# Performance work log

Hardware: AMD Instinct MI355X
Metric: run time of the kernel (lower is better)

## Reference

```python
import math
import jax, jax.numpy as jnp
import numpy as np

SR = 22050
FRAME_SIZE = 1025
MAX_FILTER_SIZE = 20
B, T = 16, 2048


def _build_transform_matrix(frame_size=FRAME_SIZE, sr=SR, max_filter_size=MAX_FILTER_SIZE):
    max_freq = sr / 2
    freq = np.linspace(0, max_freq, num=frame_size, endpoint=True)
    mel = 2595 * np.log10(1 + freq / 700)
    min_mel, max_mel = mel[0], mel[-1]
    raw = (mel - min_mel) / (max_mel - min_mel) * (max_filter_size - 1) + 1
    mtx = np.zeros((frame_size, frame_size), dtype=np.float32)
    for i in range(frame_size):
        fs = math.floor(raw[i]) // 2 * 2 + 1
        start, end = i - fs // 2, i + fs // 2 + 1
        start, end = max(0, start), min(end, frame_size)
        mtx[i, start:end] = 1.0 / (end - start)
    return jnp.asarray(mtx)


def setup_inputs() -> dict:
    key = jax.random.key(0)
    k1, k2 = jax.random.split(key)
    model_output = jax.random.normal(k1, (B, FRAME_SIZE, T), dtype=jnp.float32)
    target = jax.random.normal(k2, (B, FRAME_SIZE, T), dtype=jnp.float32)
    transform_matrix = _build_transform_matrix()
    return {"model_output": model_output, "target": target, "transform_matrix": transform_matrix}


def reference(model_output, target, transform_matrix):
    # db_to_amp(x)**2 == (10**(x/20))**2 == 10**(x/10)
    mo = jnp.power(10.0, model_output / 10.0)
    tg = jnp.power(10.0, target / 10.0)
    diff = mo - tg  # [B, F, T]
    # mel-scale variable-width mean filter applied as dense matmul, per original
    filtered = jnp.einsum('ij,bjt->bit', transform_matrix, diff)
    return jnp.mean(filtered ** 2)
```

## Files before the change

kernel.cpp:

```cpp
#include <hip/hip_runtime.h>


#define F 1025
#define TT 2048
#define BB 16
#define NSEG 8
#define SEG 129
#define RING 24
#define TPB 256
#define TCH 512
#define NTB (TT / TCH)
#define NBLK (BB * NTB * NSEG)
#define CHUNK 4
#define HALF 10

__global__ __launch_bounds__(TPB, 2) void mel_mse_kernel(const float* __restrict__ mo,
                                                         const float* __restrict__ tg,
                                                         const float* __restrict__ mtx,
                                                         double* __restrict__ partial) {
    const int tid = threadIdx.x;
    const int blk = blockIdx.x;
    const int s  = blk % NSEG;
    const int r_ = blk / NSEG;
    const int tb = r_ % NTB;
    const int b  = r_ / NTB;

    const int i0 = s * SEG;
    const int i1 = (i0 + SEG < F) ? (i0 + SEG) : F;
    const int nrows = i1 - i0;

    __shared__ float2 ring[RING * TPB];
    __shared__ int    be_l[SEG];
    __shared__ int    bs_l[SEG];
    __shared__ float  binv_l[SEG];

    for (int k = tid; k < nrows; k += TPB) {
        const int i  = i0 + k;
        const int c0 = (i - HALF > 0) ? (i - HALF) : 0;
        const int c1 = (i + HALF + 1 < F) ? (i + HALF + 1) : F;
        const float* mrow = mtx + (size_t)i * F;
        int first = -1, last = -1;
        float fv = 0.0f;
        for (int c = c0; c < c1; ++c) {
            const float v = mrow[c];
            if (v != 0.0f) {
                if (first < 0) { first = c; fv = v; }
                last = c;
            }
        }
        bs_l[k]   = first;
        be_l[k]   = last + 1;
        binv_l[k] = fv;
    }
    __syncthreads();

    const int jstart = bs_l[0];
    const int jend   = be_l[nrows - 1];

    const int ct = tb * TPB + tid;
    const float2* __restrict__ moP = (const float2*)(mo + (size_t)b * F * TT) + ct;
    const float2* __restrict__ tgP = (const float2*)(tg + (size_t)b * F * TT) + ct;
    const size_t rs = TT / 2;

    const float C = 0.33219281f;

    float2 A0[CHUNK], G0[CHUNK], A1[CHUNK], G1[CHUNK], A2[CHUNK], G2[CHUNK];

#define LOADC(Ad, Gd, jbase)                                        \
    _Pragma("unroll")                                               \
    for (int r = 0; r < CHUNK; ++r) {                               \
        int jr = (jbase) + r;                                       \
        jr = (jr < jend) ? jr : (jend - 1);                         \
        Ad[r] = moP[(size_t)jr * rs];                               \
        Gd[r] = tgP[(size_t)jr * rs];                               \
    }

    LOADC(A0, G0, jstart)
    LOADC(A1, G1, jstart + CHUNK)

    float wx = 0.0f, wy = 0.0f, acc = 0.0f;
    int i = 0, cs = jstart, wp = 0, rp = 0;

    for (int j = jstart; j < jend; j += CHUNK) {
        LOADC(A2, G2, j + 2 * CHUNK)
        #pragma unroll
        for (int r = 0; r < CHUNK; ++r) {
            if (j + r < jend) {
                const float dx = __builtin_amdgcn_exp2f(A0[r].x * C)
                               - __builtin_amdgcn_exp2f(G0[r].x * C);
                const float dy = __builtin_amdgcn_exp2f(A0[r].y * C)
                               - __builtin_amdgcn_exp2f(G0[r].y * C);
                float2 dv; dv.x = dx; dv.y = dy;
                ring[wp + tid] = dv;
                wp += TPB; if (wp == RING * TPB) wp = 0;
                wx += dx; wy += dy;
                while (i < nrows && be_l[i] <= j + r + 1) {
                    const int si = bs_l[i];
                    while (cs < si) {
                        const float2 o = ring[rp + tid];
                        rp += TPB; if (rp == RING * TPB) rp = 0;
                        wx -= o.x; wy -= o.y;
                        ++cs;
                    }
                    const float inv = binv_l[i];
                    const float fx = wx * inv, fy = wy * inv;
                    acc = fmaf(fx, fx, fmaf(fy, fy, acc));
                    ++i;
                }
            }
        }
        #pragma unroll
        for (int r = 0; r < CHUNK; ++r) {
            A0[r] = A1[r]; G0[r] = G1[r];
            A1[r] = A2[r]; G1[r] = G2[r];
        }
    }
#undef LOADC

    #pragma unroll
    for (int off = 32; off > 0; off >>= 1)
        acc += __shfl_down(acc, off, 64);

    __shared__ double wred[4];
    const int wid = tid >> 6, lane = tid & 63;
    if (lane == 0) wred[wid] = (double)acc;
    __syncthreads();
    if (tid == 0)
        partial[blk] = wred[0] + wred[1] + wred[2] + wred[3];
}

__global__ __launch_bounds__(256) void final_kernel(const double* __restrict__ partial,
                                                    float* __restrict__ out) {
    const int tid = threadIdx.x;
    double s = 0.0;
    for (int k = tid; k < NBLK; k += 256) s += partial[k];
    #pragma unroll
    for (int off = 32; off > 0; off >>= 1)
        s += __shfl_down(s, off, 64);
    __shared__ double wred[4];
    const int wid = tid >> 6, lane = tid & 63;
    if (lane == 0) wred[wid] = s;
    __syncthreads();
    if (tid == 0) {
        double tot = wred[0] + wred[1] + wred[2] + wred[3];
        out[0] = (float)(tot / ((double)BB * (double)F * (double)TT));
    }
}

extern "C" void kernel_launch(void* const* d_in, const int* in_sizes, int n_in,
                              void* d_out, int out_size, void* d_ws, size_t ws_size,
                              hipStream_t stream) {
    const float* mo  = (const float*)d_in[0];
    const float* tg  = (const float*)d_in[1];
    const float* mtx = (const float*)d_in[2];

    double* partial = (double*)d_ws;

    mel_mse_kernel<<<NBLK, TPB, 0, stream>>>(mo, tg, mtx, partial);
    final_kernel<<<1, 256, 0, stream>>>(partial, (float*)d_out);
}
```

Measured before the change: 68.40 us.

## Process one time column per thread instead of float2 pairs

Switches each thread from two adjacent time columns (float2) to a single column. This doubles the block count and halves the ring buffer's shared memory. The launch bound goes from 2 to 4 blocks per CU to raise occupancy and memory-level parallelism. In exchange, loads become 4-byte instead of 8-byte, and the per-row loop control and band-table setup are duplicated across twice as many blocks.

```diff
diff --git a/kernel.cpp b/kernel.cpp
--- a/kernel.cpp
+++ b/kernel.cpp
@@ -8,13 +8,12 @@
 #define SEG 129
 #define RING 24
 #define TPB 256
-#define TCH 512
-#define NTB (TT / TCH)
+#define NTB (TT / TPB)
 #define NBLK (BB * NTB * NSEG)
 #define CHUNK 4
 #define HALF 10
 
-__global__ __launch_bounds__(TPB, 2) void mel_mse_kernel(const float* __restrict__ mo,
+__global__ __launch_bounds__(TPB, 4) void mel_mse_kernel(const float* __restrict__ mo,
                                                          const float* __restrict__ tg,
                                                          const float* __restrict__ mtx,
                                                          double* __restrict__ partial) {
@@ -29,13 +28,13 @@
     const int i1 = (i0 + SEG < F) ? (i0 + SEG) : F;
     const int nrows = i1 - i0;
 
-    __shared__ float2 ring[RING * TPB];
-    __shared__ int    be_l[SEG];
-    __shared__ int    bs_l[SEG];
-    __shared__ float  binv_l[SEG];
+    __shared__ float ring[RING * TPB];
+    __shared__ int   be_l[SEG];
+    __shared__ int   bs_l[SEG];
+    __shared__ float binv_l[SEG];
 
-    for (int k = tid; k < nrows; k += TPB) {
-        const int i  = i0 + k;
+    if (tid < nrows) {
+        const int i  = i0 + tid;
         const int c0 = (i - HALF > 0) ? (i - HALF) : 0;
         const int c1 = (i + HALF + 1 < F) ? (i + HALF + 1) : F;
         const float* mrow = mtx + (size_t)i * F;
@@ -48,23 +47,23 @@
                 last = c;
             }
         }
-        bs_l[k]   = first;
-        be_l[k]   = last + 1;
-        binv_l[k] = fv;
+        bs_l[tid]   = first;
+        be_l[tid]   = last + 1;
+        binv_l[tid] = fv;
     }
     __syncthreads();
 
     const int jstart = bs_l[0];
     const int jend   = be_l[nrows - 1];
 
-    const int ct = tb * TPB + tid;
-    const float2* __restrict__ moP = (const float2*)(mo + (size_t)b * F * TT) + ct;
-    const float2* __restrict__ tgP = (const float2*)(tg + (size_t)b * F * TT) + ct;
-    const size_t rs = TT / 2;
+    const int t = tb * TPB + tid;
+    const float* __restrict__ moP = mo + (size_t)b * F * TT + t;
+    const float* __restrict__ tgP = tg + (size_t)b * F * TT + t;
+    const size_t rs = TT;
 
     const float C = 0.33219281f;
 
-    float2 A0[CHUNK], G0[CHUNK], A1[CHUNK], G1[CHUNK], A2[CHUNK], G2[CHUNK];
+    float A0[CHUNK], G0[CHUNK], A1[CHUNK], G1[CHUNK], A2[CHUNK], G2[CHUNK];
 
 #define LOADC(Ad, Gd, jbase)                                        \
     _Pragma("unroll")                                               \
@@ -78,7 +77,7 @@
     LOADC(A0, G0, jstart)
     LOADC(A1, G1, jstart + CHUNK)
 
-    float wx = 0.0f, wy = 0.0f, acc = 0.0f;
+    float wsum = 0.0f, acc = 0.0f;
     int i = 0, cs = jstart, wp = 0, rp = 0;
 
     for (int j = jstart; j < jend; j += CHUNK) {
@@ -86,25 +85,20 @@
         #pragma unroll
         for (int r = 0; r < CHUNK; ++r) {
             if (j + r < jend) {
-                const float dx = __builtin_amdgcn_exp2f(A0[r].x * C)
-                               - __builtin_amdgcn_exp2f(G0[r].x * C);
-                const float dy = __builtin_amdgcn_exp2f(A0[r].y * C)
-                               - __builtin_amdgcn_exp2f(G0[r].y * C);
-                float2 dv; dv.x = dx; dv.y = dy;
-                ring[wp + tid] = dv;
+                const float d = __builtin_amdgcn_exp2f(A0[r] * C)
+                              - __builtin_amdgcn_exp2f(G0[r] * C);
+                ring[wp + tid] = d;
                 wp += TPB; if (wp == RING * TPB) wp = 0;
-                wx += dx; wy += dy;
+                wsum += d;
                 while (i < nrows && be_l[i] <= j + r + 1) {
                     const int si = bs_l[i];
                     while (cs < si) {
-                        const float2 o = ring[rp + tid];
+                        wsum -= ring[rp + tid];
                         rp += TPB; if (rp == RING * TPB) rp = 0;
-                        wx -= o.x; wy -= o.y;
                         ++cs;
                     }
-                    const float inv = binv_l[i];
-                    const float fx = wx * inv, fy = wy * inv;
-                    acc = fmaf(fx, fx, fmaf(fy, fy, acc));
+                    const float f = wsum * binv_l[i];
+                    acc = fmaf(f, f, acc);
                     ++i;
                 }
             }
```

New measurement: 70.44 us. 3.0% more time.
